# Performance work log

Hardware: AMD Instinct MI355X
Metric: run time of the kernel (lower is better)

The kernel has to match this reference:

```python
import jax, jax.numpy as jnp
import numpy as np
import math

N, DM, DK, DV, KWIN = 500, 2048, 2048, 2048, 10

def _xavier(key, shape):
    fan_out, fan_in = shape[0], shape[1]
    limit = math.sqrt(6.0 / (fan_in + fan_out))
    return jax.random.uniform(key, (shape[0], shape[1]), jnp.float32, -limit, limit)

def setup_inputs() -> dict:
    key = jax.random.key(0)
    ks = jax.random.split(key, 7)
    X = jax.random.normal(ks[0], (N, DM), jnp.float32)
    mask = jax.random.randint(ks[1], (N, N), 0, 2, jnp.int32)
    # torch Linear weight is (out, in); store transposed so fwd is X @ W
    Wq = _xavier(ks[2], (DK, DM)).T  # [DM, DK]
    Wk = _xavier(ks[3], (DK, DM)).T
    Wv = _xavier(ks[4], (DV, DM)).T
    Wo = _xavier(ks[5], (DM, DV)).T  # [DV, DM]
    wk = _xavier(ks[6], (2 * KWIN + 1, DM))  # relative-position embedding table
    return {"X": X, "mask": mask, "Wq": Wq, "Wk": Wk, "Wv": Wv, "Wo": Wo, "wk": wk}

def reference(X, mask, Wq, Wk, Wv, Wo, wk):
    n = X.shape[0]
    scale = 1.0 / math.sqrt(DK)
    Q = X @ Wq            # [n, dk]
    K = X @ Wk            # [n, dk]
    V = X @ Wv            # [n, dv]
    Qs = Q * scale
    S = Qs @ K.T          # [n, n] content scores
    # relative-position bias: Sr[i,j] = Qs[i] . wk[clip(j-i,-k,k)+k]
    # (Shaw-style gather; identical math to wk[table] matmul, no [n,n,dm] intermediate)
    idx = jnp.clip(jnp.arange(n)[None, :] - jnp.arange(n)[:, None], -KWIN, KWIN) + KWIN  # [n, n]
    QR = Qs @ wk.T                                   # [n, 2k+1]
    Sr = jnp.take_along_axis(QR, idx, axis=1)        # [n, n]
    S = S + Sr
    S = jnp.where(mask == 0, jnp.float32(-1e9), S)
    A = jax.nn.softmax(S, axis=-1)                   # dropout_rate=0 -> identity
    Y = (A @ V) @ Wo                                 # [n, dm]
    return (Y, A)
```

## Files before the change

kernel.cpp:

```cpp
#include <hip/hip_runtime.h>
#include <hip/hip_bf16.h>


#define N_TOK 500
#define MP 512
#define DM 2048
#define KWIN_ 10
#define NREL 21

typedef __hip_bfloat16 bf16;
typedef __attribute__((ext_vector_type(8))) short short8;
typedef __attribute__((ext_vector_type(4))) float floatx4;

#define NQK 2097152L
#define NVT 1048576L
#define NS 262144L
#define NY 1048576L

__device__ inline float bfj(const short8& v, int j) {
  return __bfloat162float(((const bf16*)&v)[j]);
}

__global__ __launch_bounds__(256) void prep(
    const float* __restrict__ Wq, const float* __restrict__ Wk,
    const float* __restrict__ Wv, const float* __restrict__ Wo,
    const float* __restrict__ X, const float* __restrict__ wk,
    bf16* __restrict__ WqkT, bf16* __restrict__ WvT, bf16* __restrict__ WoT,
    bf16* __restrict__ Xb, bf16* __restrict__ wkb) {
  int z = blockIdx.z;
  int tid = threadIdx.x;
  if (z == 4) {
    int row = blockIdx.y * 32 + blockIdx.x;
    int c0 = tid * 8;
    bf16 v[8];
    if (row < MP) {
      if (row < N_TOK) {
        const float* p = X + (long)row * DM + c0;
#pragma unroll
        for (int j = 0; j < 8; ++j) v[j] = __float2bfloat16(p[j]);
      } else {
#pragma unroll
        for (int j = 0; j < 8; ++j) v[j] = __float2bfloat16(0.f);
      }
      *(short8*)(Xb + (long)row * DM + c0) = *(short8*)v;
    } else if (row < MP + NREL) {
      int r = row - MP;
      const float* p = wk + (long)r * DM + c0;
#pragma unroll
      for (int j = 0; j < 8; ++j) v[j] = __float2bfloat16(p[j]);
      *(short8*)(wkb + (long)r * DM + c0) = *(short8*)v;
    }
    return;
  }
  const float* W = (z == 0) ? Wq : (z == 1) ? Wk : (z == 2) ? Wv : Wo;
  bf16* Out = (z == 0) ? WqkT
            : (z == 1) ? (WqkT + (long)DM * DM)
            : (z == 2) ? WvT : WoT;
  __shared__ float t[64][68];
  int k0 = blockIdx.y * 64, n0 = blockIdx.x * 64;
  int rr = tid >> 4, cc = (tid & 15) * 4;
  int gsw = cc >> 2;
#pragma unroll
  for (int p = 0; p < 4; ++p) {
    int r = rr + 16 * p;
    float4 v = *(const float4*)(W + (long)(k0 + r) * DM + n0 + cc);
    *(float4*)&t[r][(gsw ^ (r & 3)) * 4] = v;
  }
  __syncthreads();
#pragma unroll
  for (int s0 = 0; s0 < 2; ++s0) {
    int s = tid + s0 * 256;
    int n = s >> 3, c = s & 7;
    bf16 v[8];
#pragma unroll
    for (int j = 0; j < 8; ++j) {
      int rowt = c * 8 + j;
      int col = ((n >> 2) ^ (rowt & 3)) * 4 + (n & 3);
      v[j] = __float2bfloat16(t[rowt][col]);
    }
    *(short8*)(Out + (long)(n0 + n) * DM + k0 + c * 8) = *(short8*)v;
  }
}

template <int OUT>
__device__ __forceinline__ void gemm_core(
    const bf16* __restrict__ A, int lda, const bf16* __restrict__ B, int ldb,
    float* __restrict__ Cf, bf16* __restrict__ Cb, int ldc, int kStart,
    int kLen, int row0, int col0) {
  __shared__ __align__(16) bf16 As[128][32];
  __shared__ __align__(16) bf16 Bs[128][32];
  int tid = threadIdx.x;
  int lane = tid & 63, w = tid >> 6;
  int wr = (w & 1) * 64, wc = (w >> 1) * 64;
  int l16 = lane & 15, l4 = lane >> 4;
  int r1 = tid >> 2, c1 = (tid & 3) * 8;
  const bf16* Ab = A + (long)row0 * lda + kStart;
  const bf16* Bb = B + (long)col0 * ldb + kStart;
  const bf16* a1p = Ab + (long)r1 * lda + c1;
  const bf16* a2p = Ab + (long)(r1 + 64) * lda + c1;
  const bf16* b1p = Bb + (long)r1 * ldb + c1;
  const bf16* b2p = Bb + (long)(r1 + 64) * ldb + c1;
  floatx4 acc[4][4] = {};
  short8 pa0 = *(const short8*)a1p, pa1 = *(const short8*)a2p;
  short8 pb0 = *(const short8*)b1p, pb1 = *(const short8*)b2p;
  for (int k0 = 0; k0 < kLen; k0 += 32) {
    if (k0) __syncthreads();
    *(short8*)&As[r1][c1] = pa0;
    *(short8*)&As[r1 + 64][c1] = pa1;
    *(short8*)&Bs[r1][c1] = pb0;
    *(short8*)&Bs[r1 + 64][c1] = pb1;
    __syncthreads();
    int kn = k0 + 32;
    if (kn < kLen) {
      pa0 = *(const short8*)(a1p + kn);
      pa1 = *(const short8*)(a2p + kn);
      pb0 = *(const short8*)(b1p + kn);
      pb1 = *(const short8*)(b2p + kn);
    }
    short8 af[4], bg[4];
#pragma unroll
    for (int g = 0; g < 4; ++g)
      af[g] = *(short8*)&As[wr + g * 16 + l16][l4 * 8];
#pragma unroll
    for (int g = 0; g < 4; ++g)
      bg[g] = *(short8*)&Bs[wc + g * 16 + l16][l4 * 8];
#pragma unroll
    for (int g = 0; g < 4; ++g)
#pragma unroll
      for (int h = 0; h < 4; ++h)
        acc[g][h] =
            __builtin_amdgcn_mfma_f32_16x16x32_bf16(af[g], bg[h], acc[g][h], 0, 0, 0);
  }
#pragma unroll
  for (int g = 0; g < 4; ++g)
#pragma unroll
    for (int h = 0; h < 4; ++h)
#pragma unroll
      for (int i = 0; i < 4; ++i) {
        long r = row0 + wr + g * 16 + l4 * 4 + i;
        long c = col0 + wc + h * 16 + l16;
        if (OUT == 0)
          Cf[r * ldc + c] = acc[g][h][i];
        else
          Cb[r * ldc + c] = __float2bfloat16(acc[g][h][i]);
      }
}

__global__ __launch_bounds__(256, 2) void gemm_qkvt(
    const bf16* __restrict__ Xb, const bf16* __restrict__ WqkT,
    const bf16* __restrict__ WvT, float* __restrict__ QKp,
    float* __restrict__ Vtp) {
  int id = blockIdx.x;
  if (id < 256) {
    int z = id >> 7, t = id & 127;
    int col0 = (t & 31) * 128, row0 = (t >> 5) * 128;
    gemm_core<0>(Xb, DM, WqkT, DM, QKp + (long)z * NQK, nullptr, 4096,
                 z * 1024, 1024, row0, col0);
  } else {
    int id2 = id - 256;
    int z = id2 >> 6, t = id2 & 63;
    int col0 = (t & 3) * 128, row0 = (t >> 2) * 128;
    gemm_core<0>(WvT, DM, Xb, DM, Vtp + (long)z * NVT, nullptr, MP, z * 1024,
                 1024, row0, col0);
  }
}

template <int OUT>
__global__ __launch_bounds__(256, 2) void gemm_k(
    const bf16* __restrict__ A, int lda, const bf16* __restrict__ B, int ldb,
    float* __restrict__ Cf, bf16* __restrict__ Cb, int ldc, int sliceK,
    long cstride) {
  float* cf = (OUT == 0) ? Cf + (long)blockIdx.z * cstride : nullptr;
  gemm_core<OUT>(A, lda, B, ldb, cf, Cb, ldc, blockIdx.z * sliceK, sliceK,
                 blockIdx.y * 128, blockIdx.x * 128);
}

__global__ __launch_bounds__(256) void reduce_qkvt(
    const float* __restrict__ QKp, const float* __restrict__ Vtp,
    bf16* __restrict__ QKbf, bf16* __restrict__ Vtb) {
  long e = ((long)blockIdx.x * 256 + threadIdx.x) * 8;
  const float* p0;
  long stride;
  bf16* out;
  long eo;
  if (e < NQK) {
    p0 = QKp + e; stride = NQK; out = QKbf; eo = e;
  } else {
    eo = e - NQK; p0 = Vtp + eo; stride = NVT; out = Vtb;
  }
  float4 a0 = *(const float4*)p0, a1 = *(const float4*)(p0 + 4);
  float4 b0 = *(const float4*)(p0 + stride), b1 = *(const float4*)(p0 + stride + 4);
  bf16 v[8];
  v[0] = __float2bfloat16(a0.x + b0.x); v[1] = __float2bfloat16(a0.y + b0.y);
  v[2] = __float2bfloat16(a0.z + b0.z); v[3] = __float2bfloat16(a0.w + b0.w);
  v[4] = __float2bfloat16(a1.x + b1.x); v[5] = __float2bfloat16(a1.y + b1.y);
  v[6] = __float2bfloat16(a1.z + b1.z); v[7] = __float2bfloat16(a1.w + b1.w);
  *(short8*)(out + eo) = *(short8*)v;
}

__global__ __launch_bounds__(256) void reduce_y(const float* __restrict__ Yp,
                                                float* __restrict__ Yout) {
  long e = (long)blockIdx.x * 2048 + threadIdx.x * 8;
  float4 a0 = *(const float4*)(Yp + e), a1 = *(const float4*)(Yp + e + 4);
  float4 b0 = *(const float4*)(Yp + NY + e), b1 = *(const float4*)(Yp + NY + e + 4);
  float4 o0 = {a0.x + b0.x, a0.y + b0.y, a0.z + b0.z, a0.w + b0.w};
  float4 o1 = {a1.x + b1.x, a1.y + b1.y, a1.z + b1.z, a1.w + b1.w};
  *(float4*)(Yout + e) = o0;
  *(float4*)(Yout + e + 4) = o1;
}

__global__ __launch_bounds__(256) void softmax_qr(
    const float* __restrict__ Sp, const bf16* __restrict__ QKbf,
    const bf16* __restrict__ wkb, const int* __restrict__ mask,
    float* __restrict__ Aout, bf16* __restrict__ Abf) {
  int i = blockIdx.x;
  int tid = threadIdx.x;
  if (i >= N_TOK) {
    Abf[(long)i * MP + tid] = __float2bfloat16(0.f);
    Abf[(long)i * MP + tid + 256] = __float2bfloat16(0.f);
    return;
  }
  int lane = tid & 63, w = tid >> 6;
  __shared__ float sQR[24];
  __shared__ float red[4];
  short8 q[4];
#pragma unroll
  for (int s = 0; s < 4; ++s)
    q[s] = *(const short8*)(QKbf + (long)i * 4096 + s * 512 + lane * 8);
  for (int r = w; r < NREL; r += 4) {
    float p = 0.f;
#pragma unroll
    for (int s = 0; s < 4; ++s) {
      short8 wv = *(const short8*)(wkb + (long)r * DM + s * 512 + lane * 8);
#pragma unroll
      for (int j = 0; j < 8; ++j) p += bfj(q[s], j) * bfj(wv, j);
    }
#pragma unroll
    for (int o = 32; o > 0; o >>= 1) p += __shfl_down(p, o);
    if (lane == 0) sQR[r] = p;
  }
  __syncthreads();
  const float scale = 0.022097086912079608f;
  float v0, v1 = -1e30f;
  int j0 = tid, j1 = tid + 256;
  {
    float s = Sp[(long)i * MP + j0] + Sp[NS + (long)i * MP + j0] +
              Sp[2 * NS + (long)i * MP + j0] + Sp[3 * NS + (long)i * MP + j0];
    int rel = j0 - i;
    rel = rel < -KWIN_ ? -KWIN_ : (rel > KWIN_ ? KWIN_ : rel);
    s = scale * (s + sQR[rel + KWIN_]);
    if (mask[(long)i * N_TOK + j0] == 0) s = -1e9f;
    v0 = s;
  }
  if (j1 < N_TOK) {
    float s = Sp[(long)i * MP + j1] + Sp[NS + (long)i * MP + j1] +
              Sp[2 * NS + (long)i * MP + j1] + Sp[3 * NS + (long)i * MP + j1];
    int rel = j1 - i;
    rel = rel < -KWIN_ ? -KWIN_ : (rel > KWIN_ ? KWIN_ : rel);
    s = scale * (s + sQR[rel + KWIN_]);
    if (mask[(long)i * N_TOK + j1] == 0) s = -1e9f;
    v1 = s;
  }
  float mx = fmaxf(v0, v1);
#pragma unroll
  for (int o = 32; o > 0; o >>= 1) mx = fmaxf(mx, __shfl_down(mx, o));
  if (lane == 0) red[w] = mx;
  __syncthreads();
  if (tid == 0) red[0] = fmaxf(fmaxf(red[0], red[1]), fmaxf(red[2], red[3]));
  __syncthreads();
  mx = red[0];
  __syncthreads();
  float e0 = expf(v0 - mx);
  float e1 = (j1 < N_TOK) ? expf(v1 - mx) : 0.f;
  float sum = e0 + e1;
#pragma unroll
  for (int o = 32; o > 0; o >>= 1) sum += __shfl_down(sum, o);
  if (lane == 0) red[w] = sum;
  __syncthreads();
  if (tid == 0) red[0] = red[0] + red[1] + red[2] + red[3];
  __syncthreads();
  float inv = 1.f / red[0];
  float a0 = e0 * inv, a1 = e1 * inv;
  Aout[(long)i * N_TOK + j0] = a0;
  if (j1 < N_TOK) Aout[(long)i * N_TOK + j1] = a1;
  Abf[(long)i * MP + j0] = __float2bfloat16(a0);
  Abf[(long)i * MP + j1] = __float2bfloat16(a1);
}

extern "C" void kernel_launch(void* const* d_in, const int* in_sizes, int n_in,
                              void* d_out, int out_size, void* d_ws,
                              size_t ws_size, hipStream_t stream) {
  const float* X = (const float*)d_in[0];
  const int* mask = (const int*)d_in[1];
  const float* Wq = (const float*)d_in[2];
  const float* Wk = (const float*)d_in[3];
  const float* Wv = (const float*)d_in[4];
  const float* Wo = (const float*)d_in[5];
  const float* wk = (const float*)d_in[6];

  float* Yout = (float*)d_out;
  float* Aout = Yout + (long)N_TOK * DM;

  const long MB = 1 << 20;
  char* p = (char*)d_ws;
  bf16* Xb = (bf16*)p;
  bf16* WqkT = (bf16*)(p + 2 * MB);
  bf16* WvT = (bf16*)(p + 18 * MB);
  bf16* WoT = (bf16*)(p + 26 * MB);
  bf16* wkb = (bf16*)(p + 34 * MB);
  float* QKp = (float*)(p + 35 * MB);
  float* Vtp = (float*)(p + 51 * MB);
  bf16* QKbf = (bf16*)(p + 59 * MB);
  bf16* Vtb = (bf16*)(p + 63 * MB);
  float* Sp = (float*)(p + 65 * MB);
  bf16* Abf = (bf16*)(p + 69 * MB);
  bf16* AVbf = (bf16*)(p + 70 * MB);
  float* Yp = (float*)(p + 72 * MB);

  dim3 b256(256);

  prep<<<dim3(32, 32, 5), b256, 0, stream>>>(Wq, Wk, Wv, Wo, X, wk, WqkT, WvT,
                                             WoT, Xb, wkb);
  gemm_qkvt<<<dim3(384), b256, 0, stream>>>(Xb, WqkT, WvT, QKp, Vtp);
  reduce_qkvt<<<dim3(1536), b256, 0, stream>>>(QKp, Vtp, QKbf, Vtb);
  gemm_k<0><<<dim3(4, 4, 4), b256, 0, stream>>>(QKbf, 4096, QKbf + 2048, 4096,
                                                Sp, nullptr, MP, 512, NS);
  softmax_qr<<<dim3(MP), b256, 0, stream>>>(Sp, QKbf, wkb, mask, Aout, Abf);
  gemm_k<1><<<dim3(16, 4, 1), b256, 0, stream>>>(Abf, MP, Vtb, MP, nullptr,
                                                 AVbf, DM, MP, 0);
  gemm_k<0><<<dim3(16, 4, 2), b256, 0, stream>>>(AVbf, DM, WoT, DM, Yp,
                                                 nullptr, DM, 1024, NY);
  reduce_y<<<dim3(N_TOK), b256, 0, stream>>>(Yp, Yout);
}
```

Measured before the change: 193.8 us.

## Load GEMM tiles directly into LDS and drop split-K for QKV projection

The GEMM core now uses global_load_lds to copy A/B tiles straight from global memory into shared memory, replacing register prefetch and explicit LDS stores, with a barrier after compute. The QKV projection GEMM runs the full K range per block and writes bf16 directly, removing fp32 partial buffers and the separate reduction kernel. This saves memory traffic and a launch but halves the block count for that GEMM and loses the register double-buffer overlap.

```diff
diff --git a/kernel.cpp b/kernel.cpp
--- a/kernel.cpp
+++ b/kernel.cpp
@@ -12,10 +12,13 @@
 typedef __attribute__((ext_vector_type(8))) short short8;
 typedef __attribute__((ext_vector_type(4))) float floatx4;
 
-#define NQK 2097152L
-#define NVT 1048576L
 #define NS 262144L
 #define NY 1048576L
+
+#define GLOADLDS(g, l)                                        \
+  __builtin_amdgcn_global_load_lds(                           \
+      (const __attribute__((address_space(1))) void*)(g),     \
+      (__attribute__((address_space(3))) void*)(l), 16, 0, 0)
 
 __device__ inline float bfj(const short8& v, int j) {
   return __bfloat162float(((const bf16*)&v)[j]);
@@ -93,30 +96,23 @@
   int lane = tid & 63, w = tid >> 6;
   int wr = (w & 1) * 64, wc = (w >> 1) * 64;
   int l16 = lane & 15, l4 = lane >> 4;
-  int r1 = tid >> 2, c1 = (tid & 3) * 8;
-  const bf16* Ab = A + (long)row0 * lda + kStart;
-  const bf16* Bb = B + (long)col0 * ldb + kStart;
-  const bf16* a1p = Ab + (long)r1 * lda + c1;
-  const bf16* a2p = Ab + (long)(r1 + 64) * lda + c1;
-  const bf16* b1p = Bb + (long)r1 * ldb + c1;
-  const bf16* b2p = Bb + (long)(r1 + 64) * ldb + c1;
+  int srow = w * 32 + (lane >> 2);
+  int scol = (lane & 3) * 8;
+  const bf16* ga0 = A + (long)(row0 + srow) * lda + kStart + scol;
+  const bf16* ga1 = ga0 + 16 * (long)lda;
+  const bf16* gb0 = B + (long)(col0 + srow) * ldb + kStart + scol;
+  const bf16* gb1 = gb0 + 16 * (long)ldb;
+  bf16* la0 = &As[w * 32][0];
+  bf16* la1 = &As[w * 32 + 16][0];
+  bf16* lb0 = &Bs[w * 32][0];
+  bf16* lb1 = &Bs[w * 32 + 16][0];
   floatx4 acc[4][4] = {};
-  short8 pa0 = *(const short8*)a1p, pa1 = *(const short8*)a2p;
-  short8 pb0 = *(const short8*)b1p, pb1 = *(const short8*)b2p;
   for (int k0 = 0; k0 < kLen; k0 += 32) {
-    if (k0) __syncthreads();
-    *(short8*)&As[r1][c1] = pa0;
-    *(short8*)&As[r1 + 64][c1] = pa1;
-    *(short8*)&Bs[r1][c1] = pb0;
-    *(short8*)&Bs[r1 + 64][c1] = pb1;
+    GLOADLDS(ga0 + k0, la0);
+    GLOADLDS(ga1 + k0, la1);
+    GLOADLDS(gb0 + k0, lb0);
+    GLOADLDS(gb1 + k0, lb1);
     __syncthreads();
-    int kn = k0 + 32;
-    if (kn < kLen) {
-      pa0 = *(const short8*)(a1p + kn);
-      pa1 = *(const short8*)(a2p + kn);
-      pb0 = *(const short8*)(b1p + kn);
-      pb1 = *(const short8*)(b2p + kn);
-    }
     short8 af[4], bg[4];
 #pragma unroll
     for (int g = 0; g < 4; ++g)
@@ -130,6 +126,7 @@
       for (int h = 0; h < 4; ++h)
         acc[g][h] =
             __builtin_amdgcn_mfma_f32_16x16x32_bf16(af[g], bg[h], acc[g][h], 0, 0, 0);
+    __syncthreads();
   }
 #pragma unroll
   for (int g = 0; g < 4; ++g)
@@ -148,20 +145,16 @@
 
 __global__ __launch_bounds__(256, 2) void gemm_qkvt(
     const bf16* __restrict__ Xb, const bf16* __restrict__ WqkT,
-    const bf16* __restrict__ WvT, float* __restrict__ QKp,
-    float* __restrict__ Vtp) {
+    const bf16* __restrict__ WvT, bf16* __restrict__ QKbf,
+    bf16* __restrict__ Vtb) {
   int id = blockIdx.x;
-  if (id < 256) {
-    int z = id >> 7, t = id & 127;
-    int col0 = (t & 31) * 128, row0 = (t >> 5) * 128;
-    gemm_core<0>(Xb, DM, WqkT, DM, QKp + (long)z * NQK, nullptr, 4096,
-                 z * 1024, 1024, row0, col0);
+  if (id < 128) {
+    int col0 = (id & 31) * 128, row0 = (id >> 5) * 128;
+    gemm_core<1>(Xb, DM, WqkT, DM, nullptr, QKbf, 4096, 0, DM, row0, col0);
   } else {
-    int id2 = id - 256;
-    int z = id2 >> 6, t = id2 & 63;
+    int t = id - 128;
     int col0 = (t & 3) * 128, row0 = (t >> 2) * 128;
-    gemm_core<0>(WvT, DM, Xb, DM, Vtp + (long)z * NVT, nullptr, MP, z * 1024,
-                 1024, row0, col0);
+    gemm_core<1>(WvT, DM, Xb, DM, nullptr, Vtb, MP, 0, DM, row0, col0);
   }
 }
 
@@ -173,29 +166,6 @@
   float* cf = (OUT == 0) ? Cf + (long)blockIdx.z * cstride : nullptr;
   gemm_core<OUT>(A, lda, B, ldb, cf, Cb, ldc, blockIdx.z * sliceK, sliceK,
                  blockIdx.y * 128, blockIdx.x * 128);
-}
-
-__global__ __launch_bounds__(256) void reduce_qkvt(
-    const float* __restrict__ QKp, const float* __restrict__ Vtp,
-    bf16* __restrict__ QKbf, bf16* __restrict__ Vtb) {
-  long e = ((long)blockIdx.x * 256 + threadIdx.x) * 8;
-  const float* p0;
-  long stride;
-  bf16* out;
-  long eo;
-  if (e < NQK) {
-    p0 = QKp + e; stride = NQK; out = QKbf; eo = e;
-  } else {
-    eo = e - NQK; p0 = Vtp + eo; stride = NVT; out = Vtb;
-  }
-  float4 a0 = *(const float4*)p0, a1 = *(const float4*)(p0 + 4);
-  float4 b0 = *(const float4*)(p0 + stride), b1 = *(const float4*)(p0 + stride + 4);
-  bf16 v[8];
-  v[0] = __float2bfloat16(a0.x + b0.x); v[1] = __float2bfloat16(a0.y + b0.y);
-  v[2] = __float2bfloat16(a0.z + b0.z); v[3] = __float2bfloat16(a0.w + b0.w);
-  v[4] = __float2bfloat16(a1.x + b1.x); v[5] = __float2bfloat16(a1.y + b1.y);
-  v[6] = __float2bfloat16(a1.z + b1.z); v[7] = __float2bfloat16(a1.w + b1.w);
-  *(short8*)(out + eo) = *(short8*)v;
 }
 
 __global__ __launch_bounds__(256) void reduce_y(const float* __restrict__ Yp,
@@ -308,21 +278,18 @@
   bf16* WvT = (bf16*)(p + 18 * MB);
   bf16* WoT = (bf16*)(p + 26 * MB);
   bf16* wkb = (bf16*)(p + 34 * MB);
-  float* QKp = (float*)(p + 35 * MB);
-  float* Vtp = (float*)(p + 51 * MB);
-  bf16* QKbf = (bf16*)(p + 59 * MB);
-  bf16* Vtb = (bf16*)(p + 63 * MB);
-  float* Sp = (float*)(p + 65 * MB);
-  bf16* Abf = (bf16*)(p + 69 * MB);
-  bf16* AVbf = (bf16*)(p + 70 * MB);
-  float* Yp = (float*)(p + 72 * MB);
+  bf16* QKbf = (bf16*)(p + 35 * MB);
+  bf16* Vtb = (bf16*)(p + 39 * MB);
+  float* Sp = (float*)(p + 41 * MB);
+  bf16* Abf = (bf16*)(p + 45 * MB);
+  bf16* AVbf = (bf16*)(p + 46 * MB);
+  float* Yp = (float*)(p + 48 * MB);
 
   dim3 b256(256);
 
   prep<<<dim3(32, 32, 5), b256, 0, stream>>>(Wq, Wk, Wv, Wo, X, wk, WqkT, WvT,
                                              WoT, Xb, wkb);
-  gemm_qkvt<<<dim3(384), b256, 0, stream>>>(Xb, WqkT, WvT, QKp, Vtp);
-  reduce_qkvt<<<dim3(1536), b256, 0, stream>>>(QKp, Vtp, QKbf, Vtb);
+  gemm_qkvt<<<dim3(192), b256, 0, stream>>>(Xb, WqkT, WvT, QKbf, Vtb);
   gemm_k<0><<<dim3(4, 4, 4), b256, 0, stream>>>(QKbf, 4096, QKbf + 2048, 4096,
                                                 Sp, nullptr, MP, 512, NS);
   softmax_qr<<<dim3(MP), b256, 0, stream>>>(Sp, QKbf, wkb, mask, Aout, Abf);
```

Measured after the change: 206.4 us. +6.5%, slower.
